# Performance work log

Measured on AMD Instinct MI355X. Metric: run time of the kernel, lower is better.

Reference implementation:

```python
import jax, jax.numpy as jnp
import numpy as np
import math

# ---- static config (mirrors init_kwargs) ----
B, CIN, COUT = 8, 32, 32
H, W = 256, 256
RADIUS_CUTOFF = 0.03
NR, NPHI = 6, 7               # kernel_shape = [6, 7] (anisotropic basis)
K = (NR - 1) * NPHI + 1       # 36 basis functions
EPS = 1e-5                    # InstanceNorm2d eps
NEG_SLOPE = 0.2


def _disco_psi(nh, nw, r_cutoff, nr, nphi):
    """Local DISCO filter basis on an equidistant [-1,1]^2 grid.
    Returns psi [K, P, P] (float32) and half-width p (P = 2p+1).
    Piecewise-linear hat functions in radius (nr rings incl. center) times
    hat functions in angle (nphi sectors), normalized and quadrature-weighted."""
    dy = 2.0 / nh
    dx = 2.0 / nw
    p = int(math.floor(r_cutoff / min(dx, dy)))
    off_y = (np.arange(-p, p + 1) * dy)[:, None]
    off_x = (np.arange(-p, p + 1) * dx)[None, :]
    r = np.sqrt(off_x ** 2 + off_y ** 2)                 # [P, P]
    phi = np.arctan2(off_y + 0 * off_x, off_x + 0 * off_y) % (2.0 * np.pi)
    dr = r_cutoff / nr
    dphi = 2.0 * np.pi / nphi
    ker = (nr - 1) * nphi + 1
    ik = np.arange(ker)[:, None, None]                   # [K,1,1]
    ir = ((ik - 1) // nphi + 1) * dr                     # ik=0 -> ring at r=0
    iphi = ((ik - 1) % nphi) * dphi
    norm = np.pi * (r_cutoff * nr / (nr + 1)) ** 2       # 2d normalization
    rv = np.clip(1.0 - np.abs(r[None] - ir) / dr, 0.0, None) * (r[None] <= r_cutoff)
    dphi_abs = np.abs(phi[None] - iphi)
    dphi_min = np.minimum(dphi_abs, 2.0 * np.pi - dphi_abs)
    pv = np.where(ik > 0, np.clip(1.0 - dphi_min / dphi, 0.0, None), 1.0)
    q = dx * dy                                          # quadrature weight
    psi = (rv * pv) * (q / norm)
    return jnp.asarray(psi, jnp.float32), p


def _upsample2x_bilinear_align_corners(x):
    """torch nn.Upsample(scale_factor=2, mode='bilinear', align_corners=True)."""
    b, c, hi, wi = x.shape
    ho, wo = 2 * hi, 2 * wi
    ys = jnp.linspace(0.0, hi - 1.0, ho)
    y0 = jnp.clip(jnp.floor(ys), 0, hi - 2).astype(jnp.int32)
    wy = (ys - y0.astype(ys.dtype))[None, None, :, None]
    x = x[:, :, y0, :] * (1.0 - wy) + x[:, :, y0 + 1, :] * wy
    xs = jnp.linspace(0.0, wi - 1.0, wo)
    x0 = jnp.clip(jnp.floor(xs), 0, wi - 2).astype(jnp.int32)
    wx = (xs - x0.astype(xs.dtype))[None, None, None, :]
    return x[:, :, :, x0] * (1.0 - wx) + x[:, :, :, x0 + 1] * wx


def setup_inputs() -> dict:
    key = jax.random.key(0)
    k1, k2 = jax.random.split(key)
    image = jax.random.normal(k1, (B, CIN, H, W), dtype=jnp.float32)
    # DISCO learnable weights: [out_ch, in_ch, kernel_size]
    scale = 1.0 / np.sqrt(CIN * K)
    weight = jax.random.normal(k2, (COUT, CIN, K), dtype=jnp.float32) * scale
    return {"image": image, "weight": weight}


def reference(image, weight):
    x = _upsample2x_bilinear_align_corners(image)
    # 2) equidistant DISCO conv: assemble dense kernel from basis, strided conv back to (H,W)
    psi, p = _disco_psi(2 * H, 2 * W, RADIUS_CUTOFF / 2.0, NR, NPHI)   # [K,P,P]
    kernel = jnp.einsum("oik,kyx->oiyx", weight, psi)                   # [O,I,P,P]
    y = jax.lax.conv_general_dilated(
        x, kernel, window_strides=(2, 2), padding=[(p, p), (p, p)],
        dimension_numbers=("NCHW", "OIHW", "NCHW"))                     # [B,O,H,W]
    # 3) InstanceNorm2d (no affine), biased variance over spatial dims
    mean = jnp.mean(y, axis=(2, 3), keepdims=True)
    var = jnp.var(y, axis=(2, 3), keepdims=True)
    y = (y - mean) * jax.lax.rsqrt(var + EPS)
    # 4) LeakyReLU(0.2)
    return jnp.where(y >= 0, y, NEG_SLOPE * y)
```

## Files before the change

### kernel.cpp

```cpp
#include <hip/hip_runtime.h>
#include <hip/hip_bf16.h>
#include <math.h>

#define B_     8
#define CIN_   32
#define COUT_  32
#define H_     256
#define W_     256
#define K_     36
#define P_     3
#define KW_    7
#define TAPS_  49
#define NPAIR_ 25
#define EPS_   1e-5f
#define SLOPE_ 0.2f

#define PART_OFF_F   25600
#define MEANRS_OFF_F 156672

#define IMG_PLANE_B   6736
#define IMG_ROW_B     336

#define XP_ROW   304
#define XO_BASE  11552

using short8_t  = __attribute__((ext_vector_type(8)))  short;
using f32x16_t  = __attribute__((ext_vector_type(16))) float;
using f32x4_t   = __attribute__((ext_vector_type(4)))  float;

__device__ inline ushort f32_to_bf16(float f) {
    unsigned int bits = __float_as_uint(f);
    unsigned int r = (bits + 0x7FFFu + ((bits >> 16) & 1u)) >> 16;
    return (ushort)r;
}

__host__ __device__ inline int pair_tap(int pi, int tt) {
    if (pi < 21) {
        const int ky = pi / 3, c = pi % 3;
        return ky * 7 + 2 * c + tt;
    }
    const int row = 2 * (pi - 21) + tt;
    return (row <= 6) ? (row * 7 + 6) : -1;
}

__global__ __launch_bounds__(256)
void build_kernel(const float* __restrict__ weight, ushort* __restrict__ kerB) {
    __shared__ float psi_s[2][K_];
    const int f  = blockIdx.x;
    const int pi = f % NPAIR_;
    const int oc = f / NPAIR_;
    const int tid = threadIdx.x;

    if (tid < 2 * K_) {
        const int tt = tid / K_;
        const int k  = tid - tt * K_;
        const int tap = pair_tap(pi, tt);
        float val = 0.f;
        if (tap >= 0) {
            const int ky = tap / 7;
            const int kx = tap % 7;
            const double dxy   = 2.0 / 512.0;
            const double rcut  = 0.015;
            const int    nr    = 6, nphi = 7;
            const double dr    = rcut / nr;
            const double dphi  = 2.0 * M_PI / nphi;
            const double norm  = M_PI * (rcut * nr / (nr + 1)) * (rcut * nr / (nr + 1));
            const double q     = dxy * dxy;
            const double offy = (double)(ky - P_) * dxy;
            const double offx = (double)(kx - P_) * dxy;
            const double r    = sqrt(offx * offx + offy * offy);
            double phi = atan2(offy, offx);
            if (phi < 0.0) phi += 2.0 * M_PI;
            double ir, iphi;
            if (k == 0) { ir = 0.0; iphi = 0.0; }
            else        { ir = (double)((k - 1) / nphi + 1) * dr;
                          iphi = (double)((k - 1) % nphi) * dphi; }
            double rv = 1.0 - fabs(r - ir) / dr;
            rv = rv > 0.0 ? rv : 0.0;
            if (r > rcut) rv = 0.0;
            double pv = 1.0;
            if (k > 0) {
                double da = fabs(phi - iphi);
                double dm = da < (2.0 * M_PI - da) ? da : (2.0 * M_PI - da);
                pv = 1.0 - dm / dphi;
                pv = pv > 0.0 ? pv : 0.0;
            }
            val = (float)(rv * pv * q / norm);
        }
        psi_s[tt][k] = val;
    }
    __syncthreads();

    for (int e = tid; e < 512; e += 256) {
        const int lane = e >> 3;
        const int j    = e & 7;
        const int gs   = lane >> 5;
        const int n    = lane & 31;
        float s = 0.f;
        if (pair_tap(pi, gs) >= 0) {
            const int ci = oc * 8 + j;
            const float* w = weight + (size_t)(n * CIN_ + ci) * K_;
            #pragma unroll
            for (int k = 0; k < K_; ++k) s = fmaf(w[k], psi_s[gs][k], s);
        }
        kerB[((size_t)f * 64 + lane) * 8 + j] = f32_to_bf16(s);
    }
}

__global__ __launch_bounds__(512, 8)
void conv_mfma(const float* __restrict__ image,
               const ushort* __restrict__ kerB,
               float* __restrict__ out,
               float* __restrict__ partials) {
    __shared__ float  Img_s[3368];
    __shared__ ushort Xup_s[11552];
    __shared__ float  wp[8][32][2];

    const int tid  = threadIdx.x;
    const int lane = tid & 63;
    const int w    = tid >> 6;
    const int j0 = blockIdx.x * 16;
    const int i0 = blockIdx.y * 16;
    const int b  = blockIdx.z;

    const int u0 = 2 * i0 - 3;
    const int v0 = 2 * j0 - 3;
    const int R0 = i0 - 2;
    const int C0 = j0 - 2;

    const int gs  = lane >> 5;
    const int tio = (lane & 31) >> 4;
    const int tj  = lane & 15;
    const int yb0 = 4 * w + 2 * tio;

    f32x16_t acc;
    #pragma unroll
    for (int q = 0; q < 16; ++q) acc[q] = 0.f;

    char* img_bytes = (char*)Img_s;
    char* xup_bytes = (char*)Xup_s;

    if (tid < 19) {
        const short8_t z = {0,0,0,0,0,0,0,0};
        *(short8_t*)(xup_bytes + 37 * XP_ROW + tid * 16) = z;
    }

    const float* imgb = image + (size_t)(b * CIN_) * (H_ * W_);

    for (int oc = 0; oc < 4; ++oc) {
        const float* img = imgb + (size_t)(oc * 8) * (H_ * W_);
        for (int e = tid; e < 800; e += 512) {
            const int p  = (e >= 400) ? 1 : 0;
            const int yx = e - p * 400;
            const int py = yx / 20, px = yx - py * 20;
            const int row = R0 + py, col = C0 + px;
            f32x4_t g = {0.f, 0.f, 0.f, 0.f};
            if ((unsigned)row < 256u && (unsigned)col < 256u) {
                const float* q = img + (size_t)p * 4 * (H_ * W_) + row * W_ + col;
                g[0] = q[0];
                g[1] = q[H_ * W_];
                g[2] = q[2 * (H_ * W_)];
                g[3] = q[3 * (H_ * W_)];
            }
            *(f32x4_t*)(img_bytes + p * IMG_PLANE_B + (py * 21 + px) * 16) = g;
        }
        __syncthreads();

        for (int e = tid; e < 703; e += 512) {
            const int y   = e / 19;
            const int xp  = e - 19 * y;
            const int x   = 2 * xp;
            const int ry  = y >> 1;
            const float wy =
                (float)((((y & 1) ? 510 : 255)) - (R0 + ry)) * (1.0f / 511.0f);
            const int Ax = C0 + xp;
            const float wx0 = (float)(255 - Ax) * (1.0f / 511.0f);
            const float wx1 = (float)(510 - Ax) * (1.0f / 511.0f);
            const bool oky = ((unsigned)(u0 + y) < 512u);
            const bool ok0 = oky && ((unsigned)(v0 + x) < 512u);
            const bool ok1 = oky && ((unsigned)(v0 + x + 1) < 512u) && (xp < 18);

            const char* lo = img_bytes + (ry * 21 + xp) * 16;
            const char* hi = lo + IMG_PLANE_B;
            const f32x4_t a00 = *(const f32x4_t*)(lo);
            const f32x4_t a01 = *(const f32x4_t*)(lo + 16);
            const f32x4_t a10 = *(const f32x4_t*)(lo + IMG_ROW_B);
            const f32x4_t a11 = *(const f32x4_t*)(lo + IMG_ROW_B + 16);
            const f32x4_t b00 = *(const f32x4_t*)(hi);
            const f32x4_t b01 = *(const f32x4_t*)(hi + 16);
            const f32x4_t b10 = *(const f32x4_t*)(hi + IMG_ROW_B);
            const f32x4_t b11 = *(const f32x4_t*)(hi + IMG_ROW_B + 16);

            const f32x4_t cA0 = a00 + wy * (a10 - a00);
            const f32x4_t cA1 = a01 + wy * (a11 - a01);
            const f32x4_t cB0 = b00 + wy * (b10 - b00);
            const f32x4_t cB1 = b01 + wy * (b11 - b01);

            {
                const f32x4_t va = cA0 + wx0 * (cA1 - cA0);
                const f32x4_t vb = cB0 + wx0 * (cB1 - cB0);
                __hip_bfloat162 h0 = __float22bfloat162_rn(make_float2(va[0], va[1]));
                __hip_bfloat162 h1 = __float22bfloat162_rn(make_float2(va[2], va[3]));
                __hip_bfloat162 h2 = __float22bfloat162_rn(make_float2(vb[0], vb[1]));
                __hip_bfloat162 h3 = __float22bfloat162_rn(make_float2(vb[2], vb[3]));
                union { short8_t s8; uint4 u4; } pk;
                pk.u4.x = ok0 ? *(unsigned int*)&h0 : 0u;
                pk.u4.y = ok0 ? *(unsigned int*)&h1 : 0u;
                pk.u4.z = ok0 ? *(unsigned int*)&h2 : 0u;
                pk.u4.w = ok0 ? *(unsigned int*)&h3 : 0u;
                *(short8_t*)(xup_bytes + y * XP_ROW + xp * 16) = pk.s8;
            }
            {
                const f32x4_t va = cA0 + wx1 * (cA1 - cA0);
                const f32x4_t vb = cB0 + wx1 * (cB1 - cB0);
                __hip_bfloat162 h0 = __float22bfloat162_rn(make_float2(va[0], va[1]));
                __hip_bfloat162 h1 = __float22bfloat162_rn(make_float2(va[2], va[3]));
                __hip_bfloat162 h2 = __float22bfloat162_rn(make_float2(vb[0], vb[1]));
                __hip_bfloat162 h3 = __float22bfloat162_rn(make_float2(vb[2], vb[3]));
                union { short8_t s8; uint4 u4; } pk;
                pk.u4.x = ok1 ? *(unsigned int*)&h0 : 0u;
                pk.u4.y = ok1 ? *(unsigned int*)&h1 : 0u;
                pk.u4.z = ok1 ? *(unsigned int*)&h2 : 0u;
                pk.u4.w = ok1 ? *(unsigned int*)&h3 : 0u;
                *(short8_t*)(xup_bytes + XO_BASE + y * XP_ROW + xp * 16) = pk.s8;
            }
        }
        __syncthreads();

        const ushort* kbp = kerB + ((size_t)(oc * NPAIR_) * 64 + lane) * 8;
        const int baseA = (gs ? XO_BASE : 0) + yb0 * XP_ROW + tj * 16;
        const int baseB = (yb0 + gs) * XP_ROW + (tj + 3) * 16;

        __builtin_amdgcn_s_setprio(1);
        #pragma unroll
        for (int ky = 0; ky < KW_; ++ky) {
            short8_t bf0 = *(const short8_t*)(kbp + (size_t)((ky * 3 + 0) * 512));
            short8_t bf1 = *(const short8_t*)(kbp + (size_t)((ky * 3 + 1) * 512));
            short8_t bf2 = *(const short8_t*)(kbp + (size_t)((ky * 3 + 2) * 512));
            const int rbase = baseA + ky * XP_ROW;
            const short8_t a0 = *(const short8_t*)(xup_bytes + rbase);
            acc = __builtin_amdgcn_mfma_f32_32x32x16_bf16(a0, bf0, acc, 0, 0, 0);
            const short8_t a1 = *(const short8_t*)(xup_bytes + rbase + 16);
            acc = __builtin_amdgcn_mfma_f32_32x32x16_bf16(a1, bf1, acc, 0, 0, 0);
            const short8_t a2 = *(const short8_t*)(xup_bytes + rbase + 32);
            acc = __builtin_amdgcn_mfma_f32_32x32x16_bf16(a2, bf2, acc, 0, 0, 0);
        }
        #pragma unroll
        for (int q = 0; q < 4; ++q) {
            const short8_t bfq =
                *(const short8_t*)(kbp + (size_t)((21 + q) * 512));
            const short8_t aq =
                *(const short8_t*)(xup_bytes + baseB + q * (2 * XP_ROW));
            acc = __builtin_amdgcn_mfma_f32_32x32x16_bf16(aq, bfq, acc, 0, 0, 0);
        }
        __builtin_amdgcn_s_setprio(0);
        if (oc != 3) __syncthreads();
    }

    const int n = lane & 31;
    float* op = out + (size_t)(b * COUT_ + n) * (H_ * W_);
    const int ibase = i0 + 2 * w;
    #pragma unroll
    for (int grp = 0; grp < 4; ++grp) {
        const int ti  = ibase + (grp >> 1);
        const int tjj = j0 + ((grp & 1) ? 8 : 0) + 4 * gs;
        f32x4_t s;
        s[0] = acc[grp * 4 + 0]; s[1] = acc[grp * 4 + 1];
        s[2] = acc[grp * 4 + 2]; s[3] = acc[grp * 4 + 3];
        *(f32x4_t*)(op + (size_t)ti * W_ + tjj) = s;
    }

    float s1 = 0.f, s2 = 0.f;
    #pragma unroll
    for (int q = 0; q < 16; ++q) { s1 += acc[q]; s2 = fmaf(acc[q], acc[q], s2); }
    s1 += __shfl_xor(s1, 32);
    s2 += __shfl_xor(s2, 32);
    if (lane < 32) { wp[w][lane][0] = s1; wp[w][lane][1] = s2; }
    __syncthreads();
    if (tid < 32) {
        float t1 = 0.f, t2 = 0.f;
        #pragma unroll
        for (int wv = 0; wv < 8; ++wv) { t1 += wp[wv][tid][0]; t2 += wp[wv][tid][1]; }
        const int tile = blockIdx.y * 16 + blockIdx.x;
        float2* pp = (float2*)partials;
        pp[((b * 32 + tid) << 8) | tile] = make_float2(t1, t2);
    }
}

__global__ __launch_bounds__(64)
void stats_kernel(const float* __restrict__ partials, float* __restrict__ meanrs) {
    const int bo = blockIdx.x;
    const int l  = threadIdx.x;
    const float2* pp = (const float2*)partials + ((size_t)bo << 8);
    float s1 = 0.f, s2 = 0.f;
    #pragma unroll
    for (int k = 0; k < 4; ++k) {
        const float2 p = pp[l + 64 * k];
        s1 += p.x; s2 += p.y;
    }
    #pragma unroll
    for (int off = 32; off > 0; off >>= 1) {
        s1 += __shfl_down(s1, off);
        s2 += __shfl_down(s2, off);
    }
    if (l == 0) {
        const float inv = 1.0f / 65536.0f;
        const float m   = s1 * inv;
        const float var = s2 * inv - m * m;
        ((float2*)meanrs)[bo] = make_float2(m, 1.0f / sqrtf(var + EPS_));
    }
}

__global__ __launch_bounds__(256)
void norm2_kernel(float* __restrict__ y, const float* __restrict__ meanrs) {
    const int blk = blockIdx.x;
    const int bo  = blk >> 6;
    const float2 mr = ((const float2*)meanrs)[bo];
    const float m  = mr.x;
    const float rs = mr.y;

    const int e = blk * 256 + threadIdx.x;
    float4 v = ((const float4*)y)[e];
    v.x = (v.x - m) * rs; v.x = v.x >= 0.f ? v.x : SLOPE_ * v.x;
    v.y = (v.y - m) * rs; v.y = v.y >= 0.f ? v.y : SLOPE_ * v.y;
    v.z = (v.z - m) * rs; v.z = v.z >= 0.f ? v.z : SLOPE_ * v.z;
    v.w = (v.w - m) * rs; v.w = v.w >= 0.f ? v.w : SLOPE_ * v.w;
    ((float4*)y)[e] = v;
}

extern "C" void kernel_launch(void* const* d_in, const int* in_sizes, int n_in,
                              void* d_out, int out_size, void* d_ws, size_t ws_size,
                              hipStream_t stream) {
    const float* image  = (const float*)d_in[0];
    const float* weight = (const float*)d_in[1];
    float*  out      = (float*)d_out;
    ushort* kerB     = (ushort*)d_ws;
    float*  partials = (float*)d_ws + PART_OFF_F;
    float*  meanrs   = (float*)d_ws + MEANRS_OFF_F;

    build_kernel<<<dim3(4 * NPAIR_), dim3(256), 0, stream>>>(weight, kerB);
    conv_mfma<<<dim3(16, 16, B_), dim3(512), 0, stream>>>(image, kerB, out, partials);
    stats_kernel<<<dim3(256), dim3(64), 0, stream>>>(partials, meanrs);
    norm2_kernel<<<dim3(16384), dim3(256), 0, stream>>>(out, meanrs);
}
```

Baseline: 120.0 us.

## Prefetch next channel group's image tile into registers during MFMA stage

Restructures the per-channel-group loop so the global loads of the next 8 input channels are issued into registers before the MFMA convolution on the current group, then written to LDS afterwards. This overlaps global-memory latency with tensor-core compute and removes one barrier per iteration. In exchange it raises register pressure, which may lower occupancy or cause spills. It relies on the image tile buffer not being read during stage 3, which holds because that stage reads only the upsampled buffer.

```diff
diff --git a/kernel.cpp b/kernel.cpp
--- a/kernel.cpp
+++ b/kernel.cpp
@@ -147,25 +147,30 @@
 
     const float* imgb = image + (size_t)(b * CIN_) * (H_ * W_);
 
-    for (int oc = 0; oc < 4; ++oc) {
-        const float* img = imgb + (size_t)(oc * 8) * (H_ * W_);
-        for (int e = tid; e < 800; e += 512) {
-            const int p  = (e >= 400) ? 1 : 0;
-            const int yx = e - p * 400;
-            const int py = yx / 20, px = yx - py * 20;
-            const int row = R0 + py, col = C0 + px;
-            f32x4_t g = {0.f, 0.f, 0.f, 0.f};
-            if ((unsigned)row < 256u && (unsigned)col < 256u) {
-                const float* q = img + (size_t)p * 4 * (H_ * W_) + row * W_ + col;
-                g[0] = q[0];
-                g[1] = q[H_ * W_];
-                g[2] = q[2 * (H_ * W_)];
-                g[3] = q[3 * (H_ * W_)];
-            }
-            *(f32x4_t*)(img_bytes + p * IMG_PLANE_B + (py * 21 + px) * 16) = g;
-        }
-        __syncthreads();
-
+    auto s1_load = [&](int oc, int e) -> f32x4_t {
+        const int p  = (e >= 400) ? 1 : 0;
+        const int yx = e - p * 400;
+        const int py = yx / 20, px = yx - py * 20;
+        const int row = R0 + py, col = C0 + px;
+        f32x4_t g = {0.f, 0.f, 0.f, 0.f};
+        if ((unsigned)row < 256u && (unsigned)col < 256u) {
+            const float* q = imgb + (size_t)(oc * 8 + p * 4) * (H_ * W_)
+                           + row * W_ + col;
+            g[0] = q[0];
+            g[1] = q[H_ * W_];
+            g[2] = q[2 * (H_ * W_)];
+            g[3] = q[3 * (H_ * W_)];
+        }
+        return g;
+    };
+    auto s1_store = [&](int e, f32x4_t g) {
+        const int p  = (e >= 400) ? 1 : 0;
+        const int yx = e - p * 400;
+        const int py = yx / 20, px = yx - py * 20;
+        *(f32x4_t*)(img_bytes + p * IMG_PLANE_B + (py * 21 + px) * 16) = g;
+    };
+
+    auto stage2 = [&]() {
         for (int e = tid; e < 703; e += 512) {
             const int y   = e / 19;
             const int xp  = e - 19 * y;
@@ -225,12 +230,12 @@
                 *(short8_t*)(xup_bytes + XO_BASE + y * XP_ROW + xp * 16) = pk.s8;
             }
         }
-        __syncthreads();
-
+    };
+
+    const int baseA = (gs ? XO_BASE : 0) + yb0 * XP_ROW + tj * 16;
+    const int baseB = (yb0 + gs) * XP_ROW + (tj + 3) * 16;
+    auto stage3 = [&](int oc) {
         const ushort* kbp = kerB + ((size_t)(oc * NPAIR_) * 64 + lane) * 8;
-        const int baseA = (gs ? XO_BASE : 0) + yb0 * XP_ROW + tj * 16;
-        const int baseB = (yb0 + gs) * XP_ROW + (tj + 3) * 16;
-
         __builtin_amdgcn_s_setprio(1);
         #pragma unroll
         for (int ky = 0; ky < KW_; ++ky) {
@@ -254,7 +259,36 @@
             acc = __builtin_amdgcn_mfma_f32_32x32x16_bf16(aq, bfq, acc, 0, 0, 0);
         }
         __builtin_amdgcn_s_setprio(0);
-        if (oc != 3) __syncthreads();
+    };
+
+    {
+        f32x4_t g0 = s1_load(0, tid);
+        s1_store(tid, g0);
+        if (tid < 288) {
+            f32x4_t g1 = s1_load(0, tid + 512);
+            s1_store(tid + 512, g1);
+        }
+    }
+    __syncthreads();
+    stage2();
+    __syncthreads();
+
+    for (int oc = 0; oc < 4; ++oc) {
+        if (oc < 3) {
+            f32x4_t pf0 = s1_load(oc + 1, tid);
+            f32x4_t pf1 = {0.f, 0.f, 0.f, 0.f};
+            if (tid < 288) pf1 = s1_load(oc + 1, tid + 512);
+
+            stage3(oc);
+
+            s1_store(tid, pf0);
+            if (tid < 288) s1_store(tid + 512, pf1);
+            __syncthreads();
+            stage2();
+            __syncthreads();
+        } else {
+            stage3(oc);
+        }
     }
 
     const int n = lane & 31;
```

Result: slower. 437.6 us (+264.8%).
